# Kernel optimization log

Measured on AMD Instinct MI355X. Metric: run time of the kernel, lower is better.

The kernel has to match this reference:

```python
import jax, jax.numpy as jnp
import numpy as np

ALPHA = 5.0   # ATan surrogate sharpness
THETA = 1.0   # firing threshold
EPS = 1e-5    # BatchNorm eps

@jax.custom_vjp
def spike(x):
    # forward: heaviside; backward: ATan surrogate
    return (x >= 0.0).astype(x.dtype)

def _spike_fwd(x):
    return spike(x), x

def _spike_bwd(x, g):
    return (g * (ALPHA / 2.0) / (1.0 + (jnp.pi / 2.0 * ALPHA * x) ** 2),)

spike.defvjp(_spike_fwd, _spike_bwd)

def lif_layer(x, W, beta_p, gamma, bias, U0):
    # x: [B,T,J], W: [I,J] -> h: [B,T,I]
    h = jnp.einsum('btj,ij->bti', x, W)
    # BatchNorm1d in training mode: per-channel stats over B*T (biased var)
    mu = h.mean(axis=(0, 1))
    var = h.var(axis=(0, 1))
    h = (h - mu) * jax.lax.rsqrt(var + EPS) * gamma + bias
    beta = jax.nn.sigmoid(beta_p)  # [I]
    S0 = jnp.zeros_like(U0)

    def step(carry, xt):
        Ut, St = carry
        Ut = beta * (Ut - THETA * St) + (1.0 - beta) * xt  # soft reset
        St = spike(Ut - THETA)
        return (Ut, St), St

    _, o = jax.lax.scan(step, (U0, S0), jnp.swapaxes(h, 0, 1))  # [T,B,I]
    return jnp.swapaxes(o, 0, 1)  # [B,T,I]

def setup_inputs() -> dict:
    key = jax.random.key(0)
    B, T, J, H = 32, 1024, 1024, 2048
    ks = jax.random.split(key, 16)
    f32 = jnp.float32
    inp = {
        'x': jax.random.normal(ks[0], (B, T, J), f32),
        'W1': jax.random.normal(ks[1], (H, J), f32) / np.sqrt(J),
        'beta1': jax.random.uniform(ks[2], (H,), f32, 0.0, 4.0),
        'gamma1': jnp.ones((H,), f32),
        'bias1': jnp.zeros((H,), f32),
        'U01': jax.random.uniform(ks[3], (B, H), f32),
        'W2': jax.random.normal(ks[4], (H, H), f32) / np.sqrt(H),
        'beta2': jax.random.uniform(ks[5], (H,), f32, 0.0, 4.0),
        'gamma2': jnp.ones((H,), f32),
        'bias2': jnp.zeros((H,), f32),
        'U02': jax.random.uniform(ks[6], (B, H), f32),
        'W3': jax.random.normal(ks[7], (J, H), f32) / np.sqrt(H),
        'beta3': jax.random.uniform(ks[8], (J,), f32, 0.0, 4.0),
        'gamma3': jnp.ones((J,), f32),
        'bias3': jnp.zeros((J,), f32),
        'U03': jax.random.uniform(ks[9], (B, J), f32),
    }
    return inp

def reference(x, W1, beta1, gamma1, bias1, U01,
              W2, beta2, gamma2, bias2, U02,
              W3, beta3, gamma3, bias3, U03):
    h = lif_layer(x, W1, beta1, gamma1, bias1, U01)
    h = lif_layer(h, W2, beta2, gamma2, bias2, U02)
    h = lif_layer(h, W3, beta3, gamma3, bias3, U03)
    return h
```

## Files before the change

kernel.cpp:

```cpp
#include <hip/hip_runtime.h>
#include <hip/hip_bf16.h>
#include <cmath>

#define BB 32
#define TT 1024
#define JJ 1024
#define HH 2048
#define MM (BB * TT)
#define MHALF (MM / 2)

typedef short s8v __attribute__((ext_vector_type(8)));
typedef float f4v __attribute__((ext_vector_type(4)));
typedef unsigned int u4v __attribute__((ext_vector_type(4)));
union ABu { u4v u; s8v v; };

__device__ inline void split_bf16x3(float w, unsigned short& h,
                                    unsigned short& m, unsigned short& l) {
    __hip_bfloat16 bh = __float2bfloat16(w);
    const float fh = __bfloat162float(bh);
    const float r1 = w - fh;
    __hip_bfloat16 bm = __float2bfloat16(r1);
    const float fm = __bfloat162float(bm);
    __hip_bfloat16 bl = __float2bfloat16(r1 - fm);
    h = *(unsigned short*)&bh; m = *(unsigned short*)&bm; l = *(unsigned short*)&bl;
}

__global__ void split_w(const float* __restrict__ W,
                        unsigned short* __restrict__ ph,
                        unsigned short* __restrict__ pm,
                        unsigned short* __restrict__ pl, int n)
{
    const int i = blockIdx.x * 256 + threadIdx.x;
    if (i >= n) return;
    split_bf16x3(W[i], ph[i], pm[i], pl[i]);
}

__global__ __launch_bounds__(512) void mfma_spk_gemm(
    const unsigned long long* __restrict__ S,
    int Mstr,
    const unsigned short* __restrict__ Wh,
    const unsigned short* __restrict__ Wm,
    const unsigned short* __restrict__ Wl,
    float* __restrict__ C, int M, int N, int K)
{
    __shared__ __align__(16) unsigned short Blds[2][3][2][64][32];
    const int tid = threadIdx.x;
    const int wv = tid >> 6;
    const int lane = tid & 63;
    const int wm = wv >> 1, wn = wv & 1;
    const int r16 = lane & 15, quad = lane >> 4;
    const int bm = blockIdx.x * 512;
    const int bn = blockIdx.y * 64;
    const unsigned int q8 = quad * 8;

    f4v acc[8][2] = {};

    const int rl = lane >> 2, chl = lane & 3;
    const unsigned short* sW[3];
    size_t sOff[3];
    int sP[3], sKh[3], sQ[3];
#pragma unroll
    for (int i = 0; i < 3; ++i) {
        const int e = wv * 3 + i;
        const int p = e >> 3, kh = (e >> 2) & 1, q = e & 3;
        const int srow = q * 16 + rl;
        const int kc = (chl - (srow >> 1)) & 3;
        sW[i] = (p == 0) ? Wh : (p == 1) ? Wm : Wl;
        sOff[i] = (size_t)(bn + srow) * K + kh * 32 + kc * 8;
        sP[i] = p; sKh[i] = kh; sQ[i] = q;
    }

    size_t abase[8];
#pragma unroll
    for (int ms = 0; ms < 8; ++ms)
        abase[ms] = (size_t)(bm + wm * 128 + ms * 16 + r16);

    int bR[2], bC[2];
#pragma unroll
    for (int ns = 0; ns < 2; ++ns) {
        bR[ns] = wn * 32 + ns * 16 + r16;
        bC[ns] = ((quad + (bR[ns] >> 1)) & 3) * 8;
    }

    auto stageB = [&](int buf, int i, int k0) {
        __builtin_amdgcn_global_load_lds(
            (const __attribute__((address_space(1))) void*)(sW[i] + sOff[i] + k0),
            (__attribute__((address_space(3))) void*)&Blds[buf][sP[i]][sKh[i]][sQ[i] * 16][0],
            16, 0, 0);
    };

    const int NT = K >> 6;

    unsigned long long a64A[8], a64B[8];
#pragma unroll
    for (int ms = 0; ms < 8; ++ms) a64A[ms] = S[abase[ms]];
#pragma unroll
    for (int i = 0; i < 3; ++i) stageB(0, i, 0);
    __syncthreads();

#define SPK_STEP(CURA, NXTA, CURL, NXTL, T)                                  \
    do {                                                                     \
        if ((T) + 1 < NT) {                                                  \
            _Pragma("unroll")                                                \
            for (int i = 0; i < 3; ++i) stageB((NXTL), i, ((T) + 1) << 6);   \
            _Pragma("unroll")                                                \
            for (int ms = 0; ms < 8; ++ms)                                   \
                NXTA[ms] = S[(size_t)((T) + 1) * Mstr + abase[ms]];          \
        }                                                                    \
        s8v afr[2][8];                                                       \
        _Pragma("unroll")                                                    \
        for (int ms = 0; ms < 8; ++ms) {                                     \
            const unsigned int w0 = (unsigned int)CURA[ms];                  \
            const unsigned int w1 = (unsigned int)(CURA[ms] >> 32);          \
            _Pragma("unroll")                                                \
            for (int kh = 0; kh < 2; ++kh) {                                 \
                const unsigned int w = kh ? w1 : w0;                         \
                const unsigned int bl = (w >> q8) & 0xFu;                    \
                const unsigned int bh = (w >> (q8 + 4)) & 0xFu;              \
                const unsigned int lo = (bl * 0x00204081u) & 0x01010101u;    \
                const unsigned int hi = (bh * 0x00204081u) & 0x01010101u;    \
                ABu tu;                                                      \
                tu.u[0] = __builtin_amdgcn_perm(0u, lo, 0x04010400u) * 0x3F80u; \
                tu.u[1] = __builtin_amdgcn_perm(0u, lo, 0x04030402u) * 0x3F80u; \
                tu.u[2] = __builtin_amdgcn_perm(0u, hi, 0x04010400u) * 0x3F80u; \
                tu.u[3] = __builtin_amdgcn_perm(0u, hi, 0x04030402u) * 0x3F80u; \
                afr[kh][ms] = tu.v;                                          \
            }                                                                \
        }                                                                    \
        _Pragma("unroll")                                                    \
        for (int p = 0; p < 3; ++p)                                          \
            _Pragma("unroll")                                                \
            for (int kh = 0; kh < 2; ++kh) {                                 \
                s8v bf[2];                                                   \
                _Pragma("unroll")                                            \
                for (int ns = 0; ns < 2; ++ns)                               \
                    bf[ns] = *(const s8v*)&Blds[CURL][p][kh][bR[ns]][bC[ns]];\
                __builtin_amdgcn_s_setprio(1);                               \
                _Pragma("unroll")                                            \
                for (int ms = 0; ms < 8; ++ms)                               \
                    _Pragma("unroll")                                        \
                    for (int ns = 0; ns < 2; ++ns)                           \
                        acc[ms][ns] = __builtin_amdgcn_mfma_f32_16x16x32_bf16( \
                            afr[kh][ms], bf[ns], acc[ms][ns], 0, 0, 0);      \
                __builtin_amdgcn_s_setprio(0);                               \
            }                                                                \
        if ((T) + 1 < NT) __syncthreads();                                   \
    } while (0)

    for (int t = 0; t < NT; t += 2) {
        SPK_STEP(a64A, a64B, 0, 1, t);
        SPK_STEP(a64B, a64A, 1, 0, t + 1);
    }
#undef SPK_STEP

#pragma unroll
    for (int ms = 0; ms < 8; ++ms)
#pragma unroll
        for (int ns = 0; ns < 2; ++ns) {
            const int row = bm + wm * 128 + ms * 16 + quad * 4;
            const int col = bn + wn * 32 + ns * 16 + r16;
#pragma unroll
            for (int r = 0; r < 4; ++r)
                C[(size_t)(row + r) * N + col] = acc[ms][ns][r];
        }
}

struct Sp3 { unsigned int o0, o1, o2; };

__device__ inline Sp3 split_pair(float x, float y)
{
    const unsigned int xb = __float_as_uint(x), yb = __float_as_uint(y);
    const unsigned int x0 = xb & 0xFFFF0000u,  y0 = yb & 0xFFFF0000u;
    const float xr1 = x - __uint_as_float(x0), yr1 = y - __uint_as_float(y0);
    const unsigned int x1b = __float_as_uint(xr1), y1b = __float_as_uint(yr1);
    const unsigned int x1 = x1b & 0xFFFF0000u, y1 = y1b & 0xFFFF0000u;
    const float xr2 = xr1 - __uint_as_float(x1), yr2 = yr1 - __uint_as_float(y1);
    Sp3 r;
    r.o0 = __builtin_amdgcn_perm(yb, xb, 0x07060302u);
    r.o1 = __builtin_amdgcn_perm(y1b, x1b, 0x07060302u);
    r.o2 = __builtin_amdgcn_perm(__float_as_uint(yr2), __float_as_uint(xr2), 0x07060302u);
    return r;
}

__global__ __launch_bounds__(256) void mfma_f32x3_gemm(
    const float* __restrict__ A,
    const unsigned short* __restrict__ Wh,
    const unsigned short* __restrict__ Wm,
    const unsigned short* __restrict__ Wl,
    float* __restrict__ C, int M, int N, int K)
{
    __shared__ __align__(16) unsigned short Blds[2][3][128][32];
    const int tid = threadIdx.x;
    const int wv = tid >> 6;
    const int lane = tid & 63;
    const int wm = wv >> 1, wn = wv & 1;
    const int r16 = lane & 15, quad = lane >> 4;

    const int lin = blockIdx.y * 16 + blockIdx.x;
    const int ppx = gridDim.y >> 3;
    const int xcd = lin & 7, li = lin >> 3;
    const int pm = xcd * ppx + (li >> 4);
    const int pn = li & 15;
    const int bm = pm * 128;
    const int bn = pn * 128;

    f4v acc[4][4] = {};

    const int rl = lane >> 2, chl = lane & 3;
    size_t soff[2];
    int ldsrow[2];
#pragma unroll
    for (int i = 0; i < 2; ++i) {
        const int r = i * 64 + wv * 16 + rl;
        const int kc = (chl - (r >> 1)) & 3;
        soff[i] = (size_t)(bn + r) * K + kc * 8;
        ldsrow[i] = i * 64 + wv * 16;
    }

    size_t aoff[4];
#pragma unroll
    for (int ms = 0; ms < 4; ++ms)
        aoff[ms] = (size_t)(bm + wm * 64 + ms * 16 + r16) * K + quad * 8;

    int bR[4], bC[4];
#pragma unroll
    for (int ns = 0; ns < 4; ++ns) {
        bR[ns] = wn * 64 + ns * 16 + r16;
        bC[ns] = ((quad + (bR[ns] >> 1)) & 3) * 8;
    }

    auto stage = [&](int buf, int p, int i, int k0) {
        const unsigned short* Wp = (p == 0) ? Wh : (p == 1) ? Wm : Wl;
        __builtin_amdgcn_global_load_lds(
            (const __attribute__((address_space(1))) void*)(Wp + soff[i] + k0),
            (__attribute__((address_space(3))) void*)&Blds[buf][p][ldsrow[i]][0], 16, 0, 0);
    };

    float4 av[4][2];
#pragma unroll
    for (int ms = 0; ms < 4; ++ms) {
        av[ms][0] = *(const float4*)(A + aoff[ms]);
        av[ms][1] = *(const float4*)(A + aoff[ms] + 4);
    }
#pragma unroll
    for (int p = 0; p < 3; ++p)
#pragma unroll
        for (int i = 0; i < 2; ++i) stage(0, p, i, 0);
    __syncthreads();

    const int NT = K >> 5;
    for (int t = 0; t < NT; ++t) {
        const int cur = t & 1, nxt = cur ^ 1;
        const int k0 = t << 5;

        if (t + 1 < NT) {
#pragma unroll
            for (int p = 0; p < 3; ++p)
#pragma unroll
                for (int i = 0; i < 2; ++i) stage(nxt, p, i, k0 + 32);
        }

        s8v afr[3][4];
#pragma unroll
        for (int ms = 0; ms < 4; ++ms) {
            ABu t0, t1, t2;
            const float4 v0 = av[ms][0];
            const float4 v1 = av[ms][1];
            const Sp3 s0 = split_pair(v0.x, v0.y);
            const Sp3 s1 = split_pair(v0.z, v0.w);
            const Sp3 s2 = split_pair(v1.x, v1.y);
            const Sp3 s3 = split_pair(v1.z, v1.w);
            t0.u[0] = s0.o0; t1.u[0] = s0.o1; t2.u[0] = s0.o2;
            t0.u[1] = s1.o0; t1.u[1] = s1.o1; t2.u[1] = s1.o2;
            t0.u[2] = s2.o0; t1.u[2] = s2.o1; t2.u[2] = s2.o2;
            t0.u[3] = s3.o0; t1.u[3] = s3.o1; t2.u[3] = s3.o2;
            afr[0][ms] = t0.v;
            afr[1][ms] = t1.v;
            afr[2][ms] = t2.v;
        }
        if (t + 1 < NT) {
#pragma unroll
            for (int ms = 0; ms < 4; ++ms) {
                av[ms][0] = *(const float4*)(A + aoff[ms] + k0 + 32);
                av[ms][1] = *(const float4*)(A + aoff[ms] + k0 + 32 + 4);
            }
        }

#pragma unroll
        for (int pw = 0; pw < 3; ++pw) {
            s8v bf[4];
#pragma unroll
            for (int ns = 0; ns < 4; ++ns)
                bf[ns] = *(const s8v*)&Blds[cur][pw][bR[ns]][bC[ns]];
            __builtin_amdgcn_s_setprio(1);
#pragma unroll
            for (int pa = 0; pa + pw < 3; ++pa)
#pragma unroll
                for (int ms = 0; ms < 4; ++ms)
#pragma unroll
                    for (int ns = 0; ns < 4; ++ns)
                        acc[ms][ns] = __builtin_amdgcn_mfma_f32_16x16x32_bf16(
                            afr[pa][ms], bf[ns], acc[ms][ns], 0, 0, 0);
            __builtin_amdgcn_s_setprio(0);
        }

        if (t + 1 < NT) __syncthreads();
    }

#pragma unroll
    for (int ms = 0; ms < 4; ++ms)
#pragma unroll
        for (int ns = 0; ns < 4; ++ns) {
            const int row = bm + wm * 64 + ms * 16 + quad * 4;
            const int col = bn + wn * 64 + ns * 16 + r16;
#pragma unroll
            for (int r = 0; r < 4; ++r)
                C[(size_t)(row + r) * N + col] = acc[ms][ns][r];
        }
}

#define RCHUNK 128

__global__ void bn_stats_partial2(const float* __restrict__ hA,
                                  const float* __restrict__ hB,
                                  float* __restrict__ partial, int N)
{
    const int n = blockIdx.x * 256 + threadIdx.x;
    const int chunk = blockIdx.y;
    const int half = (MM / RCHUNK) / 2;
    const float* __restrict__ h = (chunk < half) ? hA : hB;
    const int cl = chunk & (half - 1);
    const float* p = h + (size_t)cl * RCHUNK * N + n;
    float s = 0.f, s2 = 0.f;
#pragma unroll 4
    for (int r = 0; r < RCHUNK; ++r) {
        const float v = p[(size_t)r * N];
        s += v;
        s2 = fmaf(v, v, s2);
    }
    partial[((size_t)chunk * 2 + 0) * N + n] = s;
    partial[((size_t)chunk * 2 + 1) * N + n] = s2;
}

__global__ void bn_stats_final(const float* __restrict__ partial,
                               float* __restrict__ stats,
                               int N, int nchunks)
{
    const int n = blockIdx.x * 256 + threadIdx.x;
    double s = 0.0, s2 = 0.0;
    for (int c = 0; c < nchunks; ++c) {
        s  += (double)partial[((size_t)c * 2 + 0) * N + n];
        s2 += (double)partial[((size_t)c * 2 + 1) * N + n];
    }
    const double inv_m = 1.0 / (double)MM;
    const double mu = s * inv_m;
    const double var = s2 * inv_m - mu * mu;
    stats[n]     = (float)mu;
    stats[N + n] = (float)(1.0 / sqrt(var + 1e-5));
}

#define LIF_STEP_PACK(hv)                                            \
    do {                                                             \
        const float hn = ((hv) - mu) * rstd * g + bi;                \
        u = beta * (u - s) + omb * hn;                               \
        const bool sp = (u - 1.0f) >= 0.f;                           \
        s = sp ? 1.f : 0.f;                                          \
        const unsigned long long mball = __ballot(sp);               \
        if (lead) bits[widx] = mball;                                \
        ++widx;                                                      \
    } while (0)

#define LIF_LOAD8(buf, tbase)                                        \
    _Pragma("unroll")                                                \
    for (int j = 0; j < 8; ++j) {                                    \
        const int tl = (tbase) + j;                                  \
        buf[j] = h[base + (size_t)(tl < TT ? tl : TT - 1) * N];      \
    }

__global__ __launch_bounds__(64) void bn_lif_scan_pack2(
    const float* __restrict__ hA,
    const float* __restrict__ hB,
    unsigned long long* __restrict__ bits,
    const float* __restrict__ stats,
    const float* __restrict__ gamma,
    const float* __restrict__ bias,
    const float* __restrict__ beta_p,
    const float* __restrict__ U0,
    int N)
{
    const int n = blockIdx.x * 64 + threadIdx.x;
    const int b = blockIdx.y;
    const float* __restrict__ h = (b < BB / 2) ? hA : hB;
    const int bl = b & (BB / 2 - 1);
    const float mu = stats[n];
    const float rstd = stats[N + n];
    const float g = gamma[n];
    const float bi = bias[n];
    const float beta = 1.f / (1.f + expf(-beta_p[n]));
    const float omb = 1.f - beta;
    float u = U0[(size_t)b * N + n];
    float s = 0.f;
    const size_t base = ((size_t)bl * TT) * N + n;
    size_t widx = (size_t)(n >> 6) * (size_t)MM + (size_t)b * TT;
    const bool lead = (threadIdx.x & 63) == 0;

    float b0[8], b1[8], b2[8], b3[8];
    LIF_LOAD8(b0, 0);
    LIF_LOAD8(b1, 8);
    LIF_LOAD8(b2, 16);
    for (int t0 = 0; t0 < TT; t0 += 32) {
        LIF_LOAD8(b3, t0 + 24);
#pragma unroll
        for (int j = 0; j < 8; ++j) { const float hv = b0[j]; LIF_STEP_PACK(hv); }
        LIF_LOAD8(b0, t0 + 32);
#pragma unroll
        for (int j = 0; j < 8; ++j) { const float hv = b1[j]; LIF_STEP_PACK(hv); }
        LIF_LOAD8(b1, t0 + 40);
#pragma unroll
        for (int j = 0; j < 8; ++j) { const float hv = b2[j]; LIF_STEP_PACK(hv); }
        LIF_LOAD8(b2, t0 + 48);
#pragma unroll
        for (int j = 0; j < 8; ++j) { const float hv = b3[j]; LIF_STEP_PACK(hv); }
    }
}

#define LIF_STEP_F32(hv)                                             \
    do {                                                             \
        const float hn = ((hv) - mu) * rstd * g + bi;                \
        u = beta * (u - s) + omb * hn;                               \
        s = ((u - 1.0f) >= 0.f) ? 1.f : 0.f;                         \
        out[oidx] = s;                                               \
        oidx += N;                                                   \
    } while (0)

__global__ __launch_bounds__(64) void bn_lif_scan_f32_2(
    const float* __restrict__ h,
    float* __restrict__ out,
    const float* __restrict__ stats,
    const float* __restrict__ gamma,
    const float* __restrict__ bias,
    const float* __restrict__ beta_p,
    const float* __restrict__ U0,
    int N)
{
    const int n = blockIdx.x * 64 + threadIdx.x;
    const int b = blockIdx.y;
    const float mu = stats[n];
    const float rstd = stats[N + n];
    const float g = gamma[n];
    const float bi = bias[n];
    const float beta = 1.f / (1.f + expf(-beta_p[n]));
    const float omb = 1.f - beta;
    float u = U0[(size_t)b * N + n];
    float s = 0.f;
    const size_t base = ((size_t)b * TT) * N + n;
    size_t oidx = base;

    float b0[8], b1[8], b2[8], b3[8];
    LIF_LOAD8(b0, 0);
    LIF_LOAD8(b1, 8);
    LIF_LOAD8(b2, 16);
    for (int t0 = 0; t0 < TT; t0 += 32) {
        LIF_LOAD8(b3, t0 + 24);
#pragma unroll
        for (int j = 0; j < 8; ++j) { const float hv = b0[j]; LIF_STEP_F32(hv); }
        LIF_LOAD8(b0, t0 + 32);
#pragma unroll
        for (int j = 0; j < 8; ++j) { const float hv = b1[j]; LIF_STEP_F32(hv); }
        LIF_LOAD8(b1, t0 + 40);
#pragma unroll
        for (int j = 0; j < 8; ++j) { const float hv = b2[j]; LIF_STEP_F32(hv); }
        LIF_LOAD8(b2, t0 + 48);
#pragma unroll
        for (int j = 0; j < 8; ++j) { const float hv = b3[j]; LIF_STEP_F32(hv); }
    }
}

extern "C" void kernel_launch(void* const* d_in, const int* in_sizes, int n_in,
                              void* d_out, int out_size, void* d_ws, size_t ws_size,
                              hipStream_t stream)
{
    const float* x   = (const float*)d_in[0];
    const float* W1  = (const float*)d_in[1];
    const float* bp1 = (const float*)d_in[2];
    const float* g1  = (const float*)d_in[3];
    const float* bi1 = (const float*)d_in[4];
    const float* U01 = (const float*)d_in[5];
    const float* W2  = (const float*)d_in[6];
    const float* bp2 = (const float*)d_in[7];
    const float* g2  = (const float*)d_in[8];
    const float* bi2 = (const float*)d_in[9];
    const float* U02 = (const float*)d_in[10];
    const float* W3  = (const float*)d_in[11];
    const float* bp3 = (const float*)d_in[12];
    const float* g3  = (const float*)d_in[13];
    const float* bi3 = (const float*)d_in[14];
    const float* U03 = (const float*)d_in[15];
    float* out = (float*)d_out;

    unsigned char* ws = (unsigned char*)d_ws;
    const size_t HA_BYTES  = (size_t)MHALF * HH * sizeof(float);
    const size_t SPK_BYTES = (size_t)MM * (HH / 8);
    float*              hA   = (float*)ws;
    float*              hB   = (float*)d_out;
    unsigned long long* spk  = (unsigned long long*)(ws + HA_BYTES);
    float*              part = (float*)(ws + HA_BYTES + SPK_BYTES);
    float*              stat = (float*)(ws + HA_BYTES + SPK_BYTES + 4194304);
    unsigned short*     W2h  = (unsigned short*)(ws + HA_BYTES + SPK_BYTES + 4194304 + 16384);
    unsigned short*     W2m  = W2h + (size_t)HH * HH;
    unsigned short*     W2l  = W2m + (size_t)HH * HH;
    unsigned short*     W3h  = W2l + (size_t)HH * HH;
    unsigned short*     W3m  = W3h + (size_t)JJ * HH;
    unsigned short*     W3l  = W3m + (size_t)JJ * HH;

    const dim3 blk(256);
    const dim3 blk64(64);
    const dim3 blk512(512);
    const int nck = MM / RCHUNK;

    split_w<<<dim3((HH * JJ) / 256), blk, 0, stream>>>(W1, W2h, W2m, W2l, HH * JJ);
    mfma_f32x3_gemm<<<dim3(HH / 128, MHALF / 128), blk, 0, stream>>>(
        x, W2h, W2m, W2l, hA, MHALF, HH, JJ);
    mfma_f32x3_gemm<<<dim3(HH / 128, MHALF / 128), blk, 0, stream>>>(
        x + (size_t)MHALF * JJ, W2h, W2m, W2l, hB, MHALF, HH, JJ);
    split_w<<<dim3((HH * HH) / 256), blk, 0, stream>>>(W2, W2h, W2m, W2l, HH * HH);
    split_w<<<dim3((JJ * HH) / 256), blk, 0, stream>>>(W3, W3h, W3m, W3l, JJ * HH);

    bn_stats_partial2<<<dim3(HH / 256, nck), blk, 0, stream>>>(hA, hB, part, HH);
    bn_stats_final<<<dim3(HH / 256), blk, 0, stream>>>(part, stat, HH, nck);
    bn_lif_scan_pack2<<<dim3(HH / 64, BB), blk64, 0, stream>>>(
        hA, hB, spk, stat, g1, bi1, bp1, U01, HH);

    mfma_spk_gemm<<<dim3(MHALF / 512, HH / 64), blk512, 0, stream>>>(
        spk, MM, W2h, W2m, W2l, hA, MHALF, HH, HH);
    mfma_spk_gemm<<<dim3(MHALF / 512, HH / 64), blk512, 0, stream>>>(
        spk + MHALF, MM, W2h, W2m, W2l, hB, MHALF, HH, HH);
    bn_stats_partial2<<<dim3(HH / 256, nck), blk, 0, stream>>>(hA, hB, part, HH);
    bn_stats_final<<<dim3(HH / 256), blk, 0, stream>>>(part, stat, HH, nck);
    bn_lif_scan_pack2<<<dim3(HH / 64, BB), blk64, 0, stream>>>(
        hA, hB, spk, stat, g2, bi2, bp2, U02, HH);

    mfma_spk_gemm<<<dim3(MM / 512, JJ / 64), blk512, 0, stream>>>(
        spk, MM, W3h, W3m, W3l, hA, MM, JJ, HH);
    bn_stats_partial2<<<dim3(JJ / 256, nck), blk, 0, stream>>>(
        hA, hA + (size_t)MHALF * JJ, part, JJ);
    bn_stats_final<<<dim3(JJ / 256), blk, 0, stream>>>(part, stat, JJ, nck);
    bn_lif_scan_f32_2<<<dim3(JJ / 64, BB), blk64, 0, stream>>>(
        hA, out, stat, g3, bi3, bp3, U03, JJ);
}
```

Measured before the change: 2.314 ms.

## Fuse BatchNorm partial statistics into GEMM epilogues and merge half-launches

Each GEMM epilogue now reduces per-column sum and sum-of-squares over its tile, using shuffles and LDS across waves, and writes them as partials. This removes the separate bn_stats_partial pass that reread the full fp32 activation matrix after every layer. The two half-M GEMM launches are merged into one full-M launch that routes rows to the A or B buffer. The cost is a slightly longer epilogue with two extra barriers, and statistics that come from the fp32 accumulators in a different summation order.

```diff
diff --git a/kernel.cpp b/kernel.cpp
--- a/kernel.cpp
+++ b/kernel.cpp
@@ -41,9 +41,13 @@
     const unsigned short* __restrict__ Wh,
     const unsigned short* __restrict__ Wm,
     const unsigned short* __restrict__ Wl,
-    float* __restrict__ C, int M, int N, int K)
+    float* __restrict__ CA,
+    float* __restrict__ CB,
+    float* __restrict__ part,
+    int M, int N, int K)
 {
     __shared__ __align__(16) unsigned short Blds[2][3][2][64][32];
+    __shared__ float SredS[3][2][2][32];
     const int tid = threadIdx.x;
     const int wv = tid >> 6;
     const int lane = tid & 63;
@@ -153,15 +157,54 @@
     }
 #undef SPK_STEP
 
+    float s1v[2], s2v[2];
+#pragma unroll
+    for (int ns = 0; ns < 2; ++ns) {
+        float s = 0.f, s2 = 0.f;
+#pragma unroll
+        for (int ms = 0; ms < 8; ++ms)
+#pragma unroll
+            for (int r = 0; r < 4; ++r) {
+                const float v = acc[ms][ns][r];
+                s += v;
+                s2 = fmaf(v, v, s2);
+            }
+        s += __shfl_down(s, 32);  s += __shfl_down(s, 16);
+        s2 += __shfl_down(s2, 32); s2 += __shfl_down(s2, 16);
+        s1v[ns] = s; s2v[ns] = s2;
+    }
+    __syncthreads();
+    if (wm > 0 && lane < 16) {
+#pragma unroll
+        for (int ns = 0; ns < 2; ++ns) {
+            SredS[wm - 1][wn][0][ns * 16 + lane] = s1v[ns];
+            SredS[wm - 1][wn][1][ns * 16 + lane] = s2v[ns];
+        }
+    }
+    __syncthreads();
+    if (wm == 0 && lane < 16) {
+#pragma unroll
+        for (int ns = 0; ns < 2; ++ns) {
+            const int col = bn + wn * 32 + ns * 16 + lane;
+            const int li = ns * 16 + lane;
+            const float s  = s1v[ns] + SredS[0][wn][0][li] + SredS[1][wn][0][li] + SredS[2][wn][0][li];
+            const float s2 = s2v[ns] + SredS[0][wn][1][li] + SredS[1][wn][1][li] + SredS[2][wn][1][li];
+            part[((size_t)blockIdx.x * 2 + 0) * N + col] = s;
+            part[((size_t)blockIdx.x * 2 + 1) * N + col] = s2;
+        }
+    }
+
+    float* __restrict__ CO = (bm < MHALF) ? CA : CB;
+    const int rsub = (bm < MHALF) ? 0 : MHALF;
 #pragma unroll
     for (int ms = 0; ms < 8; ++ms)
 #pragma unroll
         for (int ns = 0; ns < 2; ++ns) {
-            const int row = bm + wm * 128 + ms * 16 + quad * 4;
+            const int row = bm - rsub + wm * 128 + ms * 16 + quad * 4;
             const int col = bn + wn * 32 + ns * 16 + r16;
 #pragma unroll
             for (int r = 0; r < 4; ++r)
-                C[(size_t)(row + r) * N + col] = acc[ms][ns][r];
+                CO[(size_t)(row + r) * N + col] = acc[ms][ns][r];
         }
 }
 
@@ -187,9 +230,13 @@
     const unsigned short* __restrict__ Wh,
     const unsigned short* __restrict__ Wm,
     const unsigned short* __restrict__ Wl,
-    float* __restrict__ C, int M, int N, int K)
+    float* __restrict__ CA,
+    float* __restrict__ CB,
+    float* __restrict__ part,
+    int M, int N, int K)
 {
     __shared__ __align__(16) unsigned short Blds[2][3][128][32];
+    __shared__ float SredF[2][2][64];
     const int tid = threadIdx.x;
     const int wv = tid >> 6;
     const int lane = tid & 63;
@@ -307,40 +354,56 @@
         if (t + 1 < NT) __syncthreads();
     }
 
+    float s1v[4], s2v[4];
+#pragma unroll
+    for (int ns = 0; ns < 4; ++ns) {
+        float s = 0.f, s2 = 0.f;
+#pragma unroll
+        for (int ms = 0; ms < 4; ++ms)
+#pragma unroll
+            for (int r = 0; r < 4; ++r) {
+                const float v = acc[ms][ns][r];
+                s += v;
+                s2 = fmaf(v, v, s2);
+            }
+        s += __shfl_down(s, 32);  s += __shfl_down(s, 16);
+        s2 += __shfl_down(s2, 32); s2 += __shfl_down(s2, 16);
+        s1v[ns] = s; s2v[ns] = s2;
+    }
+    __syncthreads();
+    if (wm == 1 && lane < 16) {
+#pragma unroll
+        for (int ns = 0; ns < 4; ++ns) {
+            SredF[wn][0][ns * 16 + lane] = s1v[ns];
+            SredF[wn][1][ns * 16 + lane] = s2v[ns];
+        }
+    }
+    __syncthreads();
+    if (wm == 0 && lane < 16) {
+#pragma unroll
+        for (int ns = 0; ns < 4; ++ns) {
+            const int col = bn + wn * 64 + ns * 16 + lane;
+            const int li = ns * 16 + lane;
+            part[((size_t)pm * 2 + 0) * N + col] = s1v[ns] + SredF[wn][0][li];
+            part[((size_t)pm * 2 + 1) * N + col] = s2v[ns] + SredF[wn][1][li];
+        }
+    }
+
+    float* __restrict__ CO = (bm < MHALF) ? CA : CB;
+    const int rsub = (bm < MHALF) ? 0 : MHALF;
 #pragma unroll
     for (int ms = 0; ms < 4; ++ms)
 #pragma unroll
         for (int ns = 0; ns < 4; ++ns) {
-            const int row = bm + wm * 64 + ms * 16 + quad * 4;
+            const int row = bm - rsub + wm * 64 + ms * 16 + quad * 4;
             const int col = bn + wn * 64 + ns * 16 + r16;
 #pragma unroll
             for (int r = 0; r < 4; ++r)
-                C[(size_t)(row + r) * N + col] = acc[ms][ns][r];
+                CO[(size_t)(row + r) * N + col] = acc[ms][ns][r];
         }
 }
 
 #define RCHUNK 128
-
-__global__ void bn_stats_partial2(const float* __restrict__ hA,
-                                  const float* __restrict__ hB,
-                                  float* __restrict__ partial, int N)
-{
-    const int n = blockIdx.x * 256 + threadIdx.x;
-    const int chunk = blockIdx.y;
-    const int half = (MM / RCHUNK) / 2;
-    const float* __restrict__ h = (chunk < half) ? hA : hB;
-    const int cl = chunk & (half - 1);
-    const float* p = h + (size_t)cl * RCHUNK * N + n;
-    float s = 0.f, s2 = 0.f;
-#pragma unroll 4
-    for (int r = 0; r < RCHUNK; ++r) {
-        const float v = p[(size_t)r * N];
-        s += v;
-        s2 = fmaf(v, v, s2);
-    }
-    partial[((size_t)chunk * 2 + 0) * N + n] = s;
-    partial[((size_t)chunk * 2 + 1) * N + n] = s2;
-}
 
 __global__ void bn_stats_final(const float* __restrict__ partial,
                                float* __restrict__ stats,
@@ -516,35 +579,26 @@
     const dim3 blk(256);
     const dim3 blk64(64);
     const dim3 blk512(512);
-    const int nck = MM / RCHUNK;
 
     split_w<<<dim3((HH * JJ) / 256), blk, 0, stream>>>(W1, W2h, W2m, W2l, HH * JJ);
-    mfma_f32x3_gemm<<<dim3(HH / 128, MHALF / 128), blk, 0, stream>>>(
-        x, W2h, W2m, W2l, hA, MHALF, HH, JJ);
-    mfma_f32x3_gemm<<<dim3(HH / 128, MHALF / 128), blk, 0, stream>>>(
-        x + (size_t)MHALF * JJ, W2h, W2m, W2l, hB, MHALF, HH, JJ);
+    mfma_f32x3_gemm<<<dim3(HH / 128, MM / 128), blk, 0, stream>>>(
+        x, W2h, W2m, W2l, hA, hB, part, MM, HH, JJ);
     split_w<<<dim3((HH * HH) / 256), blk, 0, stream>>>(W2, W2h, W2m, W2l, HH * HH);
     split_w<<<dim3((JJ * HH) / 256), blk, 0, stream>>>(W3, W3h, W3m, W3l, JJ * HH);
 
-    bn_stats_partial2<<<dim3(HH / 256, nck), blk, 0, stream>>>(hA, hB, part, HH);
-    bn_stats_final<<<dim3(HH / 256), blk, 0, stream>>>(part, stat, HH, nck);
+    bn_stats_final<<<dim3(HH / 256), blk, 0, stream>>>(part, stat, HH, MM / 128);
     bn_lif_scan_pack2<<<dim3(HH / 64, BB), blk64, 0, stream>>>(
         hA, hB, spk, stat, g1, bi1, bp1, U01, HH);
 
-    mfma_spk_gemm<<<dim3(MHALF / 512, HH / 64), blk512, 0, stream>>>(
-        spk, MM, W2h, W2m, W2l, hA, MHALF, HH, HH);
-    mfma_spk_gemm<<<dim3(MHALF / 512, HH / 64), blk512, 0, stream>>>(
-        spk + MHALF, MM, W2h, W2m, W2l, hB, MHALF, HH, HH);
-    bn_stats_partial2<<<dim3(HH / 256, nck), blk, 0, stream>>>(hA, hB, part, HH);
-    bn_stats_final<<<dim3(HH / 256), blk, 0, stream>>>(part, stat, HH, nck);
+    mfma_spk_gemm<<<dim3(MM / 512, HH / 64), blk512, 0, stream>>>(
+        spk, MM, W2h, W2m, W2l, hA, hB, part, MM, HH, HH);
+    bn_stats_final<<<dim3(HH / 256), blk, 0, stream>>>(part, stat, HH, MM / 512);
     bn_lif_scan_pack2<<<dim3(HH / 64, BB), blk64, 0, stream>>>(
         hA, hB, spk, stat, g2, bi2, bp2, U02, HH);
 
     mfma_spk_gemm<<<dim3(MM / 512, JJ / 64), blk512, 0, stream>>>(
-        spk, MM, W3h, W3m, W3l, hA, MM, JJ, HH);
-    bn_stats_partial2<<<dim3(JJ / 256, nck), blk, 0, stream>>>(
-        hA, hA + (size_t)MHALF * JJ, part, JJ);
-    bn_stats_final<<<dim3(JJ / 256), blk, 0, stream>>>(part, stat, JJ, nck);
+        spk, MM, W3h, W3m, W3l, hA, hA + (size_t)MHALF * JJ, part, MM, JJ, HH);
+    bn_stats_final<<<dim3(JJ / 256), blk, 0, stream>>>(part, stat, JJ, MM / 512);
     bn_lif_scan_f32_2<<<dim3(JJ / 64, BB), blk64, 0, stream>>>(
         hA, out, stat, g3, bi3, bp3, U03, JJ);
 }
```

Measured after the change: 2.253 ms (median of 2 runs). -2.6%, faster.
